# Kernel tuning notes

Measured on AMD Instinct MI355X. Metric: run time of the kernel, lower is better.

## Reference

```python
import jax, jax.numpy as jnp
import numpy as np

MAX_DIM = 1024
VOCAB = 257
DEPTH = 6
Q_DIM = MAX_DIM // 4  # 256
EXP_DIMS = [1, 2, 4, 8, 16, 32, 64, 128]  # expander sizes: current_q doubles up to Q_DIM
BATCH, SEQ = 8, 4096


def qlinear(q, W):
    """Quaternion Hamilton-product linear.
    q: [..., in, 4] (last dim = r,i,j,k components), W: [4, out, in] (stacked r,i,j,k weights).
    Returns [..., out, 4].
    """
    # P[..., o, w, a] = F.linear(component_a, W_w)  -> all 16 small GEMMs in one einsum
    P = jnp.einsum('...ia,woi->...owa', q, W)
    Pr, Pi, Pj, Pk = P[..., 0, :], P[..., 1, :], P[..., 2, :], P[..., 3, :]  # each [..., out, 4]
    out_r = Pr[..., 0] - Pi[..., 1] - Pj[..., 2] - Pk[..., 3]
    out_i = Pi[..., 0] + Pr[..., 1] + Pk[..., 2] - Pj[..., 3]
    out_j = Pj[..., 0] - Pk[..., 1] + Pr[..., 2] + Pi[..., 3]
    out_k = Pk[..., 0] + Pj[..., 1] - Pi[..., 2] + Pr[..., 3]
    return jnp.stack([out_r, out_i, out_j, out_k], axis=-1)


def qnormalize(q):
    norm = jnp.linalg.norm(q, axis=-1, keepdims=True)
    return q / (norm + 1e-8)


def setup_inputs() -> dict:
    key = jax.random.key(0)
    ks = jax.random.split(key, 4 + len(EXP_DIMS))
    inp = {}
    inp['x'] = jax.random.randint(ks[0], (BATCH, SEQ), 0, VOCAB)
    inp['emb'] = jax.random.normal(ks[1], (VOCAB, 4), dtype=jnp.float32)
    for idx, cq in enumerate(EXP_DIMS):
        scale = cq ** (-0.5)
        inp[f'w_exp{idx}'] = jax.random.uniform(ks[2 + idx], (4, cq, cq), jnp.float32, -scale, scale)
    scale = Q_DIM ** (-0.5)
    inp['w_layers'] = jax.random.uniform(ks[-2], (DEPTH, 4, Q_DIM, Q_DIM), jnp.float32, -scale, scale)
    inp['w_head'] = jax.random.normal(ks[-1], (VOCAB, MAX_DIM), dtype=jnp.float32) * MAX_DIM ** (-0.5)
    return inp


def reference(x, emb, w_exp0, w_exp1, w_exp2, w_exp3, w_exp4, w_exp5, w_exp6, w_exp7,
              w_layers, w_head):
    q = emb[x][:, :, None, :]  # [B, S, 1, 4]
    for w in (w_exp0, w_exp1, w_exp2, w_exp3, w_exp4, w_exp5, w_exp6, w_exp7):
        delta = jnp.tanh(qlinear(q, w))
        q = jnp.concatenate([q + delta, q - delta], axis=2)  # doubles quaternion dim
    for d in range(DEPTH):
        q = qnormalize(qlinear(q, w_layers[d]))
    stability_loss = jnp.mean(jnp.abs(q[..., 0]))
    h_flat = q.reshape(x.shape[0], x.shape[1], -1)  # [B, S, MAX_DIM]
    logits = jnp.einsum('bsd,vd->bsv', h_flat, w_head)
    return (logits, stability_loss)
```

## Files before the change

### kernel.cpp

```cpp
#include <hip/hip_runtime.h>


typedef _Float16 f16x8 __attribute__((ext_vector_type(8)));
typedef float    f32x4 __attribute__((ext_vector_type(4)));

#define GL2LDS16(gp, lp) __builtin_amdgcn_global_load_lds(                     \
    (const __attribute__((address_space(1))) void*)(gp),                       \
    (__attribute__((address_space(3))) void*)(lp), 16, 0, 0)

#define STG(slot, isB, half, PT, kb)                                           \
  do {                                                                         \
    GL2LDS16(PT[half][0] + (kb),                                               \
             S + (slot) * 32768 + (isB) * 16384 + (half) * 8192 + tid * 8);    \
    GL2LDS16(PT[half][1] + (kb),                                               \
             S + (slot) * 32768 + (isB) * 16384 + (half) * 8192 + 4096 +       \
                 tid * 8);                                                     \
  } while (0)

__device__ __forceinline__ unsigned short f2h(float f) {
  union { _Float16 h; unsigned short u; } c;
  c.h = (_Float16)f;
  return c.u;
}
__device__ __forceinline__ float h2f(unsigned short u) {
  union { unsigned short u; _Float16 h; } c;
  c.u = u;
  return (float)c.h;
}

__global__ __launch_bounds__(256) void expand_ham(
    const float* __restrict__ w, unsigned short* __restrict__ out,
    int cq, int kbits, int total) {
  int id = blockIdx.x * 256 + threadIdx.x;
  if (id >= total) return;
  const int K = 1 << kbits;
  const int n = id >> kbits;
  const int k = id & (K - 1);
  float val = 0.f;
  if (n < 4 * cq) {
    const int o = n >> 2, a = n & 3, i = k >> 2, b = k & 3;
    const int   comp[4][4] = {{0,1,2,3},{1,0,3,2},{2,3,0,1},{3,2,1,0}};
    const float sgn [4][4] = {{1.f,-1.f,-1.f,-1.f},{1.f,1.f,1.f,-1.f},
                              {1.f,-1.f,1.f,1.f},{1.f,1.f,-1.f,1.f}};
    val = sgn[a][b] * w[comp[a][b] * cq * cq + o * cq + i];
  }
  out[id] = f2h(val);
}

__global__ __launch_bounds__(256) void expand_ham6(
    const float* __restrict__ w, unsigned short* __restrict__ out) {
  const int id = blockIdx.x * 256 + threadIdx.x;
  const int d = id >> 20;
  const int r = id & 1048575;
  const int n = r >> 10, k = r & 1023;
  const int o = n >> 2, a = n & 3, i = k >> 2, b = k & 3;
  const int   comp[4][4] = {{0,1,2,3},{1,0,3,2},{2,3,0,1},{3,2,1,0}};
  const float sgn [4][4] = {{1.f,-1.f,-1.f,-1.f},{1.f,1.f,1.f,-1.f},
                            {1.f,-1.f,1.f,1.f},{1.f,1.f,-1.f,1.f}};
  const float val =
      sgn[a][b] * w[d * 262144 + comp[a][b] * 65536 + o * 256 + i];
  out[id] = f2h(val);
}

__global__ __launch_bounds__(256) void conv_head(
    const float* __restrict__ wh, unsigned short* __restrict__ out) {
  int id = blockIdx.x * 256 + threadIdx.x;
  int v = id >> 10, k = id & 1023;
  out[id] = f2h(v < 257 ? wh[v * 1024 + k] : 0.f);
}

template <int CQ>
__device__ __forceinline__ void exp_step(float (&q)[16][4],
                                         const float* __restrict__ w) {
  float d[CQ][4];
#pragma unroll
  for (int o = 0; o < CQ; o++) {
    float pr = 0.f, pi = 0.f, pj = 0.f, pk = 0.f;
#pragma unroll
    for (int i = 0; i < CQ; i++) {
      const float wr = w[0 * CQ * CQ + o * CQ + i];
      const float wi = w[1 * CQ * CQ + o * CQ + i];
      const float wj = w[2 * CQ * CQ + o * CQ + i];
      const float wk = w[3 * CQ * CQ + o * CQ + i];
      const float qr = q[i][0], qi = q[i][1], qj = q[i][2], qk = q[i][3];
      pr += wr * qr - wi * qi - wj * qj - wk * qk;
      pi += wi * qr + wr * qi + wk * qj - wj * qk;
      pj += wj * qr - wk * qi + wr * qj + wi * qk;
      pk += wk * qr + wj * qi - wi * qj + wr * qk;
    }
    d[o][0] = tanhf(pr); d[o][1] = tanhf(pi);
    d[o][2] = tanhf(pj); d[o][3] = tanhf(pk);
  }
#pragma unroll
  for (int o = 0; o < CQ; o++)
#pragma unroll
    for (int a = 0; a < 4; a++) {
      const float dd = d[o][a], qq = q[o][a];
      q[o][a]      = qq + dd;
      q[CQ + o][a] = qq - dd;
    }
}

__global__ __launch_bounds__(256) void embed_expand(
    const int* __restrict__ x, const float* __restrict__ emb,
    const float* __restrict__ w0, const float* __restrict__ w1,
    const float* __restrict__ w2, const float* __restrict__ w3,
    unsigned short* __restrict__ out) {
  const int t = blockIdx.x * 256 + threadIdx.x;
  float q[16][4];
  const int v = x[t];
  const float4 e = *(const float4*)(emb + v * 4);
  q[0][0] = e.x; q[0][1] = e.y; q[0][2] = e.z; q[0][3] = e.w;
  exp_step<1>(q, w0);
  exp_step<2>(q, w1);
  exp_step<4>(q, w2);
  exp_step<8>(q, w3);
  ushort4* o4 = (ushort4*)(out + (size_t)t * 64);
#pragma unroll
  for (int c = 0; c < 16; c++) {
    ushort4 u;
    u.x = f2h(q[c][0]); u.y = f2h(q[c][1]);
    u.z = f2h(q[c][2]); u.w = f2h(q[c][3]);
    o4[c] = u;
  }
}

template <int EPI>
__global__ __launch_bounds__(256) void gemm_epi(
    const unsigned short* __restrict__ W,
    const unsigned short* __restrict__ Act,
    unsigned short* __restrict__ OutB, float* __restrict__ OutF,
    int K, int Nreal, int ldout) {
  __shared__ unsigned short WtL[128 * 32];
  __shared__ unsigned short WtH[128 * 32];
  __shared__ unsigned short AtL[128 * 32];
  __shared__ unsigned short AtH[128 * 32];

  const int tid  = threadIdx.x;
  const int wave = tid >> 6;
  const int lane = tid & 63;
  const int l15  = lane & 15;
  const int quad = lane >> 4;

  const int Gx = gridDim.x;
  const int L  = blockIdx.y * Gx + blockIdx.x;
  const int j  = L & 7;
  const int s  = L >> 3;
  const int nblock = (s % Gx) * 128;
  const int mblock = (32 * j + s / Gx) * 128;
  const int wn = (wave & 1) * 64;
  const int wm = (wave >> 1) * 64;

  f32x4 acc[4][4];
  const f32x4 zero = {0.f, 0.f, 0.f, 0.f};
#pragma unroll
  for (int a = 0; a < 4; a++)
#pragma unroll
    for (int b = 0; b < 4; b++) acc[a][b] = zero;

  const int row0 = tid >> 2;
  const int sub  = tid & 3;
  const unsigned short* gW0 = W   + (size_t)(nblock + row0)      * K + sub * 8;
  const unsigned short* gW1 = W   + (size_t)(nblock + row0 + 64) * K + sub * 8;
  const unsigned short* gA0 = Act + (size_t)(mblock + row0)      * K + sub * 8;
  const unsigned short* gA1 = Act + (size_t)(mblock + row0 + 64) * K + sub * 8;
  unsigned short* lWL0 = &WtL[wave * 512];
  unsigned short* lWL1 = &WtL[2048 + wave * 512];
  unsigned short* lWH0 = &WtH[wave * 512];
  unsigned short* lWH1 = &WtH[2048 + wave * 512];
  unsigned short* lAL0 = &AtL[wave * 512];
  unsigned short* lAL1 = &AtL[2048 + wave * 512];
  unsigned short* lAH0 = &AtH[wave * 512];
  unsigned short* lAH1 = &AtH[2048 + wave * 512];

  for (int kb = 0; kb < K; kb += 64) {
    GL2LDS16(gW0 + kb,      lWL0);
    GL2LDS16(gW1 + kb,      lWL1);
    GL2LDS16(gW0 + kb + 32, lWH0);
    GL2LDS16(gW1 + kb + 32, lWH1);
    GL2LDS16(gA0 + kb,      lAL0);
    GL2LDS16(gA1 + kb,      lAL1);
    GL2LDS16(gA0 + kb + 32, lAH0);
    GL2LDS16(gA1 + kb + 32, lAH1);
    __syncthreads();

    {
      f16x8 afr[4], bfr[4];
#pragma unroll
      for (int tn = 0; tn < 4; tn++)
        afr[tn] = *(const f16x8*)&WtL[(wn + tn * 16 + l15) * 32 + quad * 8];
#pragma unroll
      for (int tm = 0; tm < 4; tm++)
        bfr[tm] = *(const f16x8*)&AtL[(wm + tm * 16 + l15) * 32 + quad * 8];
#pragma unroll
      for (int tn = 0; tn < 4; tn++)
#pragma unroll
        for (int tm = 0; tm < 4; tm++)
          acc[tn][tm] = __builtin_amdgcn_mfma_f32_16x16x32_f16(
              afr[tn], bfr[tm], acc[tn][tm], 0, 0, 0);
    }
    {
      f16x8 afr[4], bfr[4];
#pragma unroll
      for (int tn = 0; tn < 4; tn++)
        afr[tn] = *(const f16x8*)&WtH[(wn + tn * 16 + l15) * 32 + quad * 8];
#pragma unroll
      for (int tm = 0; tm < 4; tm++)
        bfr[tm] = *(const f16x8*)&AtH[(wm + tm * 16 + l15) * 32 + quad * 8];
#pragma unroll
      for (int tn = 0; tn < 4; tn++)
#pragma unroll
        for (int tm = 0; tm < 4; tm++)
          acc[tn][tm] = __builtin_amdgcn_mfma_f32_16x16x32_f16(
              afr[tn], bfr[tm], acc[tn][tm], 0, 0, 0);
    }
    __syncthreads();
  }

#pragma unroll
  for (int tn = 0; tn < 4; tn++) {
    const int n = nblock + wn + tn * 16 + quad * 4;
    if (n < Nreal) {
#pragma unroll
      for (int tm = 0; tm < 4; tm++) {
        const int token = mblock + wm + tm * 16 + l15;
        const f32x4 v = acc[tn][tm];
        const unsigned short* ip = Act + (size_t)token * K + n;
        const float i0 = h2f(ip[0]), i1 = h2f(ip[1]);
        const float i2 = h2f(ip[2]), i3 = h2f(ip[3]);
        const float d0 = tanhf(v[0]), d1 = tanhf(v[1]);
        const float d2 = tanhf(v[2]), d3 = tanhf(v[3]);
        ushort4 up, um;
        up.x = f2h(i0 + d0); up.y = f2h(i1 + d1);
        up.z = f2h(i2 + d2); up.w = f2h(i3 + d3);
        um.x = f2h(i0 - d0); um.y = f2h(i1 - d1);
        um.z = f2h(i2 - d2); um.w = f2h(i3 - d3);
        *(ushort4*)&OutB[(size_t)token * ldout + n] = up;
        *(ushort4*)&OutB[(size_t)token * ldout + Nreal + n] = um;
      }
    }
  }
}

template <int EPI>
__global__ __launch_bounds__(512, 2) void gemm_8ph(
    const unsigned short* __restrict__ W,
    const unsigned short* __restrict__ Act,
    unsigned short* __restrict__ OutB, float* __restrict__ OutF,
    int K, int NW, int ldout) {
  __shared__ unsigned short S[65536];
  __shared__ float lsum[8];

  const int tid  = threadIdx.x;
  const int wave = tid >> 6;
  const int lane = tid & 63;
  const int l15  = lane & 15;
  const int quad = lane >> 4;
  const int wr   = wave >> 2;
  const int wc   = wave & 3;

  const int Gx = gridDim.x;
  const int L  = blockIdx.y * Gx + blockIdx.x;
  const int j  = L & 7;
  const int s  = L >> 3;
  const int mblock = (j * (gridDim.y >> 3) + s / Gx) * 256;
  const int nblock = (s % Gx) * 256;
  const int NI = K >> 7;

  f32x4 acc[8][4];
  const f32x4 zero = {0.f, 0.f, 0.f, 0.f};
#pragma unroll
  for (int a = 0; a < 8; a++)
#pragma unroll
    for (int b = 0; b < 4; b++) acc[a][b] = zero;

  const int r8 = tid >> 3;
  const int s8 = (tid & 7) ^ (r8 & 7);
  const unsigned short* pW[2][2];
  const unsigned short* pB[2][2];
#pragma unroll
  for (int h = 0; h < 2; h++)
#pragma unroll
    for (int g = 0; g < 2; g++) {
      int wrow = nblock + h * 128 + g * 64 + r8;
      if (wrow >= NW) wrow = NW - 1;
      pW[h][g] = W   + (size_t)wrow * K + s8 * 8;
      pB[h][g] = Act + (size_t)(mblock + h * 128 + g * 64 + r8) * K + s8 * 8;
    }

  const int lrow = l15 * 64;
  const int ksw0 = ((quad)     ^ (l15 & 7)) * 8;
  const int ksw1 = ((4 + quad) ^ (l15 & 7)) * 8;

  STG(0, 0, 0, pW, 0);  STG(0, 0, 1, pW, 0);
  STG(0, 1, 0, pB, 0);  STG(0, 1, 1, pB, 0);
  STG(1, 1, 0, pB, 64); STG(1, 1, 1, pB, 64);
  asm volatile("s_waitcnt vmcnt(4)" ::: "memory");
  __builtin_amdgcn_s_barrier();
  __builtin_amdgcn_sched_barrier(0);

  f16x8 bfr[4][2];
  for (int i = 0; i < NI; ++i) {
    const bool nl = (i < NI - 1);
    const int kA1 = (2 * i + 1) * 64;
    const int k2  = (2 * i + 2) * 64;
    const int k3  = (2 * i + 3) * 64;
#pragma unroll
    for (int p = 0; p < 8; ++p) {
      const int q  = p & 3;
      const int sb = (p >> 2) * 32768;
      if (q == 0) {
#pragma unroll
        for (int c = 0; c < 4; ++c) {
          const unsigned short* bp = S + sb + 16384 + (wc * 64 + c * 16) * 64
                                       + lrow;
          bfr[c][0] = *(const f16x8*)(bp + ksw0);
          bfr[c][1] = *(const f16x8*)(bp + ksw1);
        }
      }
      f16x8 af[2][2];
#pragma unroll
      for (int f = 0; f < 2; ++f) {
        const unsigned short* ap = S + sb + (wr * 128 + q * 32 + f * 16) * 64
                                     + lrow;
        af[f][0] = *(const f16x8*)(ap + ksw0);
        af[f][1] = *(const f16x8*)(ap + ksw1);
      }
      if      (p == 0) { STG(1, 0, 0, pW, kA1); }
      else if (p == 1) { STG(1, 0, 1, pW, kA1); }
      else if (p == 2) { if (nl) STG(0, 1, 0, pB, k2); }
      else if (p == 3) { if (nl) STG(0, 1, 1, pB, k2); }
      else if (p == 4) { if (nl) STG(0, 0, 0, pW, k2); }
      else if (p == 5) { if (nl) STG(0, 0, 1, pW, k2); }
      else if (p == 6) { if (nl) STG(1, 1, 0, pB, k3); }
      else             { if (nl) STG(1, 1, 1, pB, k3); }

      __builtin_amdgcn_s_barrier();
      asm volatile("s_waitcnt lgkmcnt(0)" ::: "memory");
      __builtin_amdgcn_sched_barrier(0);
      __builtin_amdgcn_s_setprio(1);
#pragma unroll
      for (int f = 0; f < 2; ++f)
#pragma unroll
        for (int c = 0; c < 4; ++c) {
          acc[q * 2 + f][c] = __builtin_amdgcn_mfma_f32_16x16x32_f16(
              af[f][0], bfr[c][0], acc[q * 2 + f][c], 0, 0, 0);
          acc[q * 2 + f][c] = __builtin_amdgcn_mfma_f32_16x16x32_f16(
              af[f][1], bfr[c][1], acc[q * 2 + f][c], 0, 0, 0);
        }
      __builtin_amdgcn_s_setprio(0);

      if (p == 3) {
        if (nl) asm volatile("s_waitcnt vmcnt(4)" ::: "memory");
        else    asm volatile("s_waitcnt vmcnt(0)" ::: "memory");
        __builtin_amdgcn_s_barrier();
        __builtin_amdgcn_sched_barrier(0);
      } else if (p == 7) {
        if (nl) {
          asm volatile("s_waitcnt vmcnt(4)" ::: "memory");
          __builtin_amdgcn_s_barrier();
          __builtin_amdgcn_sched_barrier(0);
        }
      } else {
        __builtin_amdgcn_s_barrier();
      }
    }
  }

  if constexpr (EPI == 0) {
#pragma unroll
    for (int tn = 0; tn < 8; tn++) {
      const int n = nblock + wr * 128 + tn * 16 + quad * 4;
#pragma unroll
      for (int tm = 0; tm < 4; tm++) {
        const int token = mblock + wc * 64 + tm * 16 + l15;
        const f32x4 v = acc[tn][tm];
        const unsigned short* ip = Act + (size_t)token * K + n;
        const float i0 = h2f(ip[0]), i1 = h2f(ip[1]);
        const float i2 = h2f(ip[2]), i3 = h2f(ip[3]);
        const float d0 = tanhf(v[0]), d1 = tanhf(v[1]);
        const float d2 = tanhf(v[2]), d3 = tanhf(v[3]);
        ushort4 up, um;
        up.x = f2h(i0 + d0); up.y = f2h(i1 + d1);
        up.z = f2h(i2 + d2); up.w = f2h(i3 + d3);
        um.x = f2h(i0 - d0); um.y = f2h(i1 - d1);
        um.z = f2h(i2 - d2); um.w = f2h(i3 - d3);
        *(ushort4*)&OutB[(size_t)token * ldout + n] = up;
        *(ushort4*)&OutB[(size_t)token * ldout + NW + n] = um;
      }
    }
  } else if constexpr (EPI == 1 || EPI == 2) {
    float loss = 0.f;
#pragma unroll
    for (int tn = 0; tn < 8; tn++) {
      const int n = nblock + wr * 128 + tn * 16 + quad * 4;
#pragma unroll
      for (int tm = 0; tm < 4; tm++) {
        const int token = mblock + wc * 64 + tm * 16 + l15;
        const f32x4 v = acc[tn][tm];
        const float nrm =
            sqrtf(v[0] * v[0] + v[1] * v[1] + v[2] * v[2] + v[3] * v[3]);
        const float inv = 1.f / (nrm + 1e-8f);
        ushort4 u;
        u.x = f2h(v[0] * inv); u.y = f2h(v[1] * inv);
        u.z = f2h(v[2] * inv); u.w = f2h(v[3] * inv);
        *(ushort4*)&OutB[(size_t)token * 1024 + n] = u;
        if constexpr (EPI == 2) loss += fabsf(v[0] * inv);
      }
    }
    if constexpr (EPI == 2) {
#pragma unroll
      for (int off = 32; off > 0; off >>= 1) loss += __shfl_down(loss, off);
      if (lane == 0) lsum[wave] = loss;
      __syncthreads();
      if (tid == 0) {
        float t = 0.f;
#pragma unroll
        for (int w8 = 0; w8 < 8; w8++) t += lsum[w8];
        atomicAdd(OutF, t * (1.f / 8388608.f));
      }
    }
  } else {
#pragma unroll
    for (int tn = 0; tn < 8; tn++) {
      const int n = nblock + wr * 128 + tn * 16 + quad * 4;
      if (n < 257) {
#pragma unroll
        for (int tm = 0; tm < 4; tm++) {
          const int token = mblock + wc * 64 + tm * 16 + l15;
          const f32x4 v = acc[tn][tm];
#pragma unroll
          for (int r = 0; r < 4; r++)
            if (n + r < 257) OutF[(size_t)token * 257 + n + r] = v[r];
        }
      }
    }
  }
}

extern "C" void kernel_launch(void* const* d_in, const int* in_sizes, int n_in,
                              void* d_out, int out_size, void* d_ws,
                              size_t ws_size, hipStream_t stream) {
  const int*   x    = (const int*)d_in[0];
  const float* emb  = (const float*)d_in[1];
  const float* we0  = (const float*)d_in[2];
  const float* we1  = (const float*)d_in[3];
  const float* we2  = (const float*)d_in[4];
  const float* we3  = (const float*)d_in[5];
  const float* we4  = (const float*)d_in[6];
  const float* we5  = (const float*)d_in[7];
  const float* we6  = (const float*)d_in[8];
  const float* we7  = (const float*)d_in[9];
  const float* wlay = (const float*)d_in[10];
  const float* wh   = (const float*)d_in[11];
  float* out = (float*)d_out;

  char* p = (char*)d_ws;
  auto alloc = [&](size_t bytes) {
    void* r = (void*)p;
    p += (bytes + 255) & ~(size_t)255;
    return r;
  };
  unsigned short* act0 = (unsigned short*)alloc(32768ull * 1024 * 2);
  unsigned short* act1 = (unsigned short*)alloc(32768ull * 1024 * 2);
  unsigned short* E4 = (unsigned short*)alloc(128 * 64 * 2);
  unsigned short* E5 = (unsigned short*)alloc(128 * 128 * 2);
  unsigned short* E6 = (unsigned short*)alloc(256 * 256 * 2);
  unsigned short* E7 = (unsigned short*)alloc(512 * 512 * 2);
  unsigned short* EL = (unsigned short*)alloc(6ull * 1024 * 1024 * 2);
  unsigned short* WH = (unsigned short*)alloc(384 * 1024 * 2);

  hipMemsetAsync(out + 8421376, 0, 4, stream);

  expand_ham<<<dim3(8192 / 256), 256, 0, stream>>>(we4, E4, 16, 6, 128 * 64);
  expand_ham<<<dim3(16384 / 256), 256, 0, stream>>>(we5, E5, 32, 7, 128 * 128);
  expand_ham<<<dim3(65536 / 256), 256, 0, stream>>>(we6, E6, 64, 8, 256 * 256);
  expand_ham<<<dim3(262144 / 256), 256, 0, stream>>>(we7, E7, 128, 9,
                                                     512 * 512);
  expand_ham6<<<dim3(6 * 1048576 / 256), 256, 0, stream>>>(wlay, EL);
  conv_head<<<dim3(384 * 1024 / 256), 256, 0, stream>>>(wh, WH);

  embed_expand<<<dim3(128), 256, 0, stream>>>(x, emb, we0, we1, we2, we3, act0);

  gemm_epi<0><<<dim3(1, 256), 256, 0, stream>>>(E4, act0, act1, nullptr, 64,
                                                64, 128);
  gemm_epi<0><<<dim3(1, 256), 256, 0, stream>>>(E5, act1, act0, nullptr, 128,
                                                128, 256);
  gemm_8ph<0><<<dim3(1, 128), 512, 0, stream>>>(E6, act0, act1, nullptr, 256,
                                                256, 512);
  gemm_8ph<0><<<dim3(2, 128), 512, 0, stream>>>(E7, act1, act0, nullptr, 512,
                                                512, 1024);

  unsigned short* a = act0;
  unsigned short* b = act1;
  for (int d = 0; d < 5; d++) {
    gemm_8ph<1><<<dim3(4, 128), 512, 0, stream>>>(EL + (size_t)d * 1048576, a,
                                                  b, nullptr, 1024, 1024, 1024);
    unsigned short* t = a; a = b; b = t;
  }
  gemm_8ph<2><<<dim3(4, 128), 512, 0, stream>>>(EL + 5ull * 1048576, a, b,
                                                out + 8421376, 1024, 1024,
                                                1024);
  { unsigned short* t = a; a = b; b = t; }

  gemm_8ph<3><<<dim3(2, 128), 512, 0, stream>>>(WH, a, nullptr, out, 1024, 384,
                                                0);
}
```

Before: 811.4 us.

## Add smaller-tile triple-buffered GEMM for depth layers and fold expander 4 into embedding

Adds a new GEMM kernel for the six depth layers. It uses 256x128 tiles with a K-step of 32, triple-buffered LDS through direct global-to-LDS loads, and launch bounds allowing 4 blocks per CU. The grid doubles to 1024 blocks, aiming for higher occupancy and better latency hiding than the old 256x256 tile with 2 blocks per CU. Separately, the fifth expander step (CQ=16) now runs in scalar code inside the embedding kernel, which removes one GEMM launch and one round trip of the activations through memory. The cost is extra per-thread register pressure in the embedding kernel and more global loads per output for the smaller tiles.

```diff
diff --git a/kernel.cpp b/kernel.cpp
--- a/kernel.cpp
+++ b/kernel.cpp
@@ -70,7 +70,7 @@
 }
 
 template <int CQ>
-__device__ __forceinline__ void exp_step(float (&q)[16][4],
+__device__ __forceinline__ void exp_step(float (*q)[4],
                                          const float* __restrict__ w) {
   float d[CQ][4];
 #pragma unroll
@@ -101,13 +101,13 @@
     }
 }
 
-__global__ __launch_bounds__(256) void embed_expand(
+__global__ __launch_bounds__(256) void embed_expand5(
     const int* __restrict__ x, const float* __restrict__ emb,
     const float* __restrict__ w0, const float* __restrict__ w1,
     const float* __restrict__ w2, const float* __restrict__ w3,
-    unsigned short* __restrict__ out) {
+    const float* __restrict__ w4, unsigned short* __restrict__ out) {
   const int t = blockIdx.x * 256 + threadIdx.x;
-  float q[16][4];
+  float q[32][4];
   const int v = x[t];
   const float4 e = *(const float4*)(emb + v * 4);
   q[0][0] = e.x; q[0][1] = e.y; q[0][2] = e.z; q[0][3] = e.w;
@@ -115,9 +115,10 @@
   exp_step<2>(q, w1);
   exp_step<4>(q, w2);
   exp_step<8>(q, w3);
-  ushort4* o4 = (ushort4*)(out + (size_t)t * 64);
-#pragma unroll
-  for (int c = 0; c < 16; c++) {
+  exp_step<16>(q, w4);
+  ushort4* o4 = (ushort4*)(out + (size_t)t * 128);
+#pragma unroll
+  for (int c = 0; c < 32; c++) {
     ushort4 u;
     u.x = f2h(q[c][0]); u.y = f2h(q[c][1]);
     u.z = f2h(q[c][2]); u.w = f2h(q[c][3]);
@@ -125,11 +126,10 @@
   }
 }
 
-template <int EPI>
-__global__ __launch_bounds__(256) void gemm_epi(
+__global__ __launch_bounds__(256) void gemm_epi0(
     const unsigned short* __restrict__ W,
     const unsigned short* __restrict__ Act,
-    unsigned short* __restrict__ OutB, float* __restrict__ OutF,
+    unsigned short* __restrict__ OutB,
     int K, int Nreal, int ldout) {
   __shared__ unsigned short WtL[128 * 32];
   __shared__ unsigned short WtH[128 * 32];
@@ -243,13 +243,143 @@
 }
 
 template <int EPI>
+__global__ __launch_bounds__(512, 4) void gemm8p(
+    const unsigned short* __restrict__ W,
+    const unsigned short* __restrict__ Act,
+    unsigned short* __restrict__ OutB, float* __restrict__ OutF,
+    int K, int NW, int ldout) {
+  __shared__ unsigned short S[3 * 12288];
+  __shared__ float lsum[8];
+
+  const int tid  = threadIdx.x;
+  const int wave = tid >> 6;
+  const int lane = tid & 63;
+  const int l15  = lane & 15;
+  const int quad = lane >> 4;
+  const int wr   = wave >> 2;
+  const int wc   = wave & 3;
+
+  const int Gx = gridDim.x;
+  const int L  = blockIdx.y * Gx + blockIdx.x;
+  const int j  = L & 7;
+  const int s  = L >> 3;
+  const int mblock = (j * (gridDim.y >> 3) + s / Gx) * 256;
+  const int nblock = (s % Gx) * 128;
+  const int NT = K >> 5;
+
+  f32x4 acc[4][4];
+  const f32x4 zero = {0.f, 0.f, 0.f, 0.f};
+#pragma unroll
+  for (int a = 0; a < 4; a++)
+#pragma unroll
+    for (int b = 0; b < 4; b++) acc[a][b] = zero;
+
+  const int rw = tid >> 2;
+  const int sl = (tid & 3) ^ ((tid >> 3) & 3);
+  const int wrow = nblock + rw;
+  const int cwr  = wrow < NW ? wrow : NW - 1;
+  const unsigned short* sW  = W   + (size_t)cwr * K + sl * 8;
+  const unsigned short* sB0 = Act + (size_t)(mblock + rw)       * K + sl * 8;
+  const unsigned short* sB1 = Act + (size_t)(mblock + 128 + rw) * K + sl * 8;
+
+  const int swz = (quad * 8) ^ ((l15 & 6) << 2);
+
+#pragma unroll
+  for (int t = 0; t < 2; ++t) {
+    unsigned short* d = S + t * 12288 + tid * 8;
+    GL2LDS16(sW  + t * 32, d);
+    GL2LDS16(sB0 + t * 32, d + 4096);
+    GL2LDS16(sB1 + t * 32, d + 8192);
+  }
+  asm volatile("s_waitcnt vmcnt(3)" ::: "memory");
+  __builtin_amdgcn_s_barrier();
+  __builtin_amdgcn_sched_barrier(0);
+
+  int bC = 0;
+  int bS = 2;
+  for (int kt = 0; kt < NT; ++kt) {
+    const unsigned short* SA = S + bC * 12288;
+    const unsigned short* SB = SA + 4096;
+
+    f16x8 af[4], bf[4];
+#pragma unroll
+    for (int t4 = 0; t4 < 4; t4++)
+      af[t4] = *(const f16x8*)(SA + (wr * 64 + t4 * 16 + l15) * 32 + swz);
+#pragma unroll
+    for (int t4 = 0; t4 < 4; t4++)
+      bf[t4] = *(const f16x8*)(SB + (wc * 64 + t4 * 16 + l15) * 32 + swz);
+
+    if (kt + 2 < NT) {
+      const int kb = (kt + 2) * 32;
+      unsigned short* d = S + bS * 12288 + tid * 8;
+      GL2LDS16(sW  + kb, d);
+      GL2LDS16(sB0 + kb, d + 4096);
+      GL2LDS16(sB1 + kb, d + 8192);
+    }
+
+    __builtin_amdgcn_s_barrier();
+    asm volatile("s_waitcnt lgkmcnt(0)" ::: "memory");
+    __builtin_amdgcn_sched_barrier(0);
+    __builtin_amdgcn_s_setprio(1);
+#pragma unroll
+    for (int tn = 0; tn < 4; tn++)
+#pragma unroll
+      for (int tm = 0; tm < 4; tm++)
+        acc[tn][tm] = __builtin_amdgcn_mfma_f32_16x16x32_f16(
+            af[tn], bf[tm], acc[tn][tm], 0, 0, 0);
+    __builtin_amdgcn_s_setprio(0);
+
+    if (kt < NT - 1) {
+      if (kt + 2 < NT) asm volatile("s_waitcnt vmcnt(3)" ::: "memory");
+      else             asm volatile("s_waitcnt vmcnt(0)" ::: "memory");
+      __builtin_amdgcn_s_barrier();
+      __builtin_amdgcn_sched_barrier(0);
+    }
+    bC = bC == 2 ? 0 : bC + 1;
+    bS = bS == 2 ? 0 : bS + 1;
+  }
+
+  {
+    float loss = 0.f;
+#pragma unroll
+    for (int tn = 0; tn < 4; tn++) {
+      const int n = nblock + wr * 64 + tn * 16 + quad * 4;
+#pragma unroll
+      for (int tm = 0; tm < 4; tm++) {
+        const int token = mblock + wc * 64 + tm * 16 + l15;
+        const f32x4 v = acc[tn][tm];
+        const float nrm =
+            sqrtf(v[0] * v[0] + v[1] * v[1] + v[2] * v[2] + v[3] * v[3]);
+        const float inv = 1.f / (nrm + 1e-8f);
+        ushort4 u;
+        u.x = f2h(v[0] * inv); u.y = f2h(v[1] * inv);
+        u.z = f2h(v[2] * inv); u.w = f2h(v[3] * inv);
+        *(ushort4*)&OutB[(size_t)token * 1024 + n] = u;
+        if constexpr (EPI == 2) loss += fabsf(v[0] * inv);
+      }
+    }
+    if constexpr (EPI == 2) {
+#pragma unroll
+      for (int off = 32; off > 0; off >>= 1) loss += __shfl_down(loss, off);
+      if (lane == 0) lsum[wave] = loss;
+      __syncthreads();
+      if (tid == 0) {
+        float t = 0.f;
+#pragma unroll
+        for (int w8 = 0; w8 < 8; w8++) t += lsum[w8];
+        atomicAdd(OutF, t * (1.f / 8388608.f));
+      }
+    }
+  }
+}
+
+template <int EPI>
 __global__ __launch_bounds__(512, 2) void gemm_8ph(
     const unsigned short* __restrict__ W,
     const unsigned short* __restrict__ Act,
     unsigned short* __restrict__ OutB, float* __restrict__ OutF,
     int K, int NW, int ldout) {
   __shared__ unsigned short S[65536];
-  __shared__ float lsum[8];
 
   const int tid  = threadIdx.x;
   const int wave = tid >> 6;
@@ -387,37 +517,6 @@
         um.z = f2h(i2 - d2); um.w = f2h(i3 - d3);
         *(ushort4*)&OutB[(size_t)token * ldout + n] = up;
         *(ushort4*)&OutB[(size_t)token * ldout + NW + n] = um;
-      }
-    }
-  } else if constexpr (EPI == 1 || EPI == 2) {
-    float loss = 0.f;
-#pragma unroll
-    for (int tn = 0; tn < 8; tn++) {
-      const int n = nblock + wr * 128 + tn * 16 + quad * 4;
-#pragma unroll
-      for (int tm = 0; tm < 4; tm++) {
-        const int token = mblock + wc * 64 + tm * 16 + l15;
-        const f32x4 v = acc[tn][tm];
-        const float nrm =
-            sqrtf(v[0] * v[0] + v[1] * v[1] + v[2] * v[2] + v[3] * v[3]);
-        const float inv = 1.f / (nrm + 1e-8f);
-        ushort4 u;
-        u.x = f2h(v[0] * inv); u.y = f2h(v[1] * inv);
-        u.z = f2h(v[2] * inv); u.w = f2h(v[3] * inv);
-        *(ushort4*)&OutB[(size_t)token * 1024 + n] = u;
-        if constexpr (EPI == 2) loss += fabsf(v[0] * inv);
-      }
-    }
-    if constexpr (EPI == 2) {
-#pragma unroll
-      for (int off = 32; off > 0; off >>= 1) loss += __shfl_down(loss, off);
-      if (lane == 0) lsum[wave] = loss;
-      __syncthreads();
-      if (tid == 0) {
-        float t = 0.f;
-#pragma unroll
-        for (int w8 = 0; w8 < 8; w8++) t += lsum[w8];
-        atomicAdd(OutF, t * (1.f / 8388608.f));
       }
     }
   } else {
@@ -463,7 +562,6 @@
   };
   unsigned short* act0 = (unsigned short*)alloc(32768ull * 1024 * 2);
   unsigned short* act1 = (unsigned short*)alloc(32768ull * 1024 * 2);
-  unsigned short* E4 = (unsigned short*)alloc(128 * 64 * 2);
   unsigned short* E5 = (unsigned short*)alloc(128 * 128 * 2);
   unsigned short* E6 = (unsigned short*)alloc(256 * 256 * 2);
   unsigned short* E7 = (unsigned short*)alloc(512 * 512 * 2);
@@ -472,7 +570,6 @@
 
   hipMemsetAsync(out + 8421376, 0, 4, stream);
 
-  expand_ham<<<dim3(8192 / 256), 256, 0, stream>>>(we4, E4, 16, 6, 128 * 64);
   expand_ham<<<dim3(16384 / 256), 256, 0, stream>>>(we5, E5, 32, 7, 128 * 128);
   expand_ham<<<dim3(65536 / 256), 256, 0, stream>>>(we6, E6, 64, 8, 256 * 256);
   expand_ham<<<dim3(262144 / 256), 256, 0, stream>>>(we7, E7, 128, 9,
@@ -480,27 +577,24 @@
   expand_ham6<<<dim3(6 * 1048576 / 256), 256, 0, stream>>>(wlay, EL);
   conv_head<<<dim3(384 * 1024 / 256), 256, 0, stream>>>(wh, WH);
 
-  embed_expand<<<dim3(128), 256, 0, stream>>>(x, emb, we0, we1, we2, we3, act0);
-
-  gemm_epi<0><<<dim3(1, 256), 256, 0, stream>>>(E4, act0, act1, nullptr, 64,
-                                                64, 128);
-  gemm_epi<0><<<dim3(1, 256), 256, 0, stream>>>(E5, act1, act0, nullptr, 128,
-                                                128, 256);
-  gemm_8ph<0><<<dim3(1, 128), 512, 0, stream>>>(E6, act0, act1, nullptr, 256,
+  embed_expand5<<<dim3(128), 256, 0, stream>>>(x, emb, we0, we1, we2, we3, we4,
+                                               act0);
+
+  gemm_epi0<<<dim3(1, 256), 256, 0, stream>>>(E5, act0, act1, 128, 128, 256);
+  gemm_8ph<0><<<dim3(1, 128), 512, 0, stream>>>(E6, act1, act0, nullptr, 256,
                                                 256, 512);
-  gemm_8ph<0><<<dim3(2, 128), 512, 0, stream>>>(E7, act1, act0, nullptr, 512,
+  gemm_8ph<0><<<dim3(2, 128), 512, 0, stream>>>(E7, act0, act1, nullptr, 512,
                                                 512, 1024);
 
-  unsigned short* a = act0;
-  unsigned short* b = act1;
+  unsigned short* a = act1;
+  unsigned short* b = act0;
   for (int d = 0; d < 5; d++) {
-    gemm_8ph<1><<<dim3(4, 128), 512, 0, stream>>>(EL + (size_t)d * 1048576, a,
-                                                  b, nullptr, 1024, 1024, 1024);
+    gemm8p<1><<<dim3(8, 128), 512, 0, stream>>>(EL + (size_t)d * 1048576, a, b,
+                                                nullptr, 1024, 1024, 1024);
     unsigned short* t = a; a = b; b = t;
   }
-  gemm_8ph<2><<<dim3(4, 128), 512, 0, stream>>>(EL + 5ull * 1048576, a, b,
-                                                out + 8421376, 1024, 1024,
-                                                1024);
+  gemm8p<2><<<dim3(8, 128), 512, 0, stream>>>(EL + 5ull * 1048576, a, b,
+                                              out + 8421376, 1024, 1024, 1024);
   { unsigned short* t = a; a = b; b = t; }
 
   gemm_8ph<3><<<dim3(2, 128), 512, 0, stream>>>(WH, a, nullptr, out, 1024, 384,
```

Result: no change. 818.0 us (+0.8%).
